# Performance work log

Measured on AMD Instinct MI355X. Metric: run time of the kernel, lower is better.

The kernel has to match this reference:

```python
import jax, jax.numpy as jnp
import numpy as np
from jax import lax

B, C, H, W = 4, 256, 64, 64
C8 = C // 8


def _conv1x1(x, w, b):
    # x: (B,C,H,W), w: (O,C) -> (B,O,H,W)
    return jnp.einsum('bchw,oc->bohw', x, w) + b[None, :, None, None]


def setup_inputs() -> dict:
    key = jax.random.key(0)
    ks = jax.random.split(key, 9)
    s1 = 1.0 / np.sqrt(C)          # fan-in scale for 1x1 convs
    sf = 1.0 / np.sqrt(2 * C * 9)  # fan-in scale for 3x3 conv
    return {
        'front_x':     jax.random.normal(ks[0], (B, C, H, W), jnp.float32),
        'cross_x':     jax.random.normal(ks[1], (B, C, H, W), jnp.float32),
        'front_x_hat': jax.random.normal(ks[2], (B, C, H, W), jnp.float32),
        'Wq': jax.random.normal(ks[3], (C8, C), jnp.float32) * s1,
        'bq': jnp.zeros((C8,), jnp.float32),
        'Wk': jax.random.normal(ks[4], (C8, C), jnp.float32) * s1,
        'bk': jnp.zeros((C8,), jnp.float32),
        'Wv': jax.random.normal(ks[5], (C, C), jnp.float32) * s1,
        'bv': jnp.zeros((C,), jnp.float32),
        'Wf': jax.random.normal(ks[6], (C, 2 * C, 3, 3), jnp.float32) * sf,
        'bf': jnp.zeros((C,), jnp.float32),
    }


def reference(front_x, cross_x, front_x_hat, Wq, bq, Wk, bk, Wv, bv, Wf, bf):
    b, c, h, w = front_x.shape
    hw = h * w
    # projections -> (B, C/8, HW)
    q = _conv1x1(cross_x, Wq, bq).reshape(b, -1, hw)
    k = _conv1x1(front_x, Wk, bk).reshape(b, -1, hw)
    # energy[b,i,j] = <key_i, query_j>  (B, HW, HW)
    energy = jnp.einsum('bci,bcj->bij', k, q)
    front_star = jnp.max(energy, axis=1)     # (B, HW) best key score per query
    front_arg = jnp.argmax(energy, axis=1)   # (B, HW) best key index per query
    # value projection and hard gather of best-matching value per position
    v = _conv1x1(front_x_hat, Wv, bv).reshape(b, c, hw)
    T = jnp.take_along_axis(v, front_arg[:, None, :], axis=2).reshape(b, c, h, w)
    S = front_star.reshape(b, 1, h, w)
    cat = jnp.concatenate([front_x, T], axis=1)  # (B, 2C, H, W)
    res = lax.conv_general_dilated(
        cat, Wf, window_strides=(1, 1), padding='SAME',
        dimension_numbers=('NCHW', 'OIHW', 'NCHW')) + bf[None, :, None, None]
    return front_x + res * S
```

## Files before the change

### kernel.cpp

```cpp
#include <hip/hip_runtime.h>

#define Bn 4
#define Cn 256
#define C8 32
#define Hn 64
#define Wn 64
#define HWn 4096
#define PADR 80
#define ROWS (HWn + 2 * PADR)
#define MARGIN 6e-3f

typedef __bf16 bf16x8 __attribute__((ext_vector_type(8)));
typedef float floatx4 __attribute__((ext_vector_type(4)));
typedef unsigned short u16x8 __attribute__((ext_vector_type(8)));

__device__ __forceinline__ unsigned short f2bf(float f) {
  union { float f; unsigned int u; } c; c.f = f;
  unsigned int u = c.u;
  return (unsigned short)((u + 0x7FFFu + ((u >> 16) & 1u)) >> 16);
}
__device__ __forceinline__ float bf2f(unsigned short h) {
  union { unsigned int u; float f; } c; c.u = ((unsigned int)h) << 16;
  return c.f;
}
__device__ __forceinline__ void gl_lds16(const void* g, void* l) {
  __builtin_amdgcn_global_load_lds(
      (__attribute__((address_space(1))) void*)(uintptr_t)g,
      (__attribute__((address_space(3))) void*)(uintptr_t)l, 16, 0, 0);
}

__global__ void prep_w(const float* __restrict__ Wq, const float* __restrict__ Wk,
                       const float* __restrict__ Wv, const float* __restrict__ Wf,
                       float* __restrict__ Wqf, float* __restrict__ Wkf,
                       unsigned short* __restrict__ Wvb, unsigned short* __restrict__ Wfb,
                       int* __restrict__ cnt) {
  size_t t = (size_t)blockIdx.x * 256 + threadIdx.x;
  if (t == 0) cnt[0] = 0;
  if (t < 8192) {
    int o = (int)(t / 256), c = (int)(t % 256);
    Wqf[(size_t)c * 32 + o] = Wq[t];
    Wkf[(size_t)c * 32 + o] = Wk[t];
  }
  if (t < 65536) Wvb[t] = f2bf(Wv[t]);
  if (t < (size_t)9 * 256 * 512) {
    int tap = (int)(t / (256 * 512));
    int rem = (int)(t % (256 * 512));
    int o = rem / 512, ci = rem % 512;
    Wfb[t] = f2bf(Wf[((size_t)o * 512 + ci) * 9 + tap]);
  }
}

__global__ __launch_bounds__(1024) void proj_qk(
    const float* __restrict__ cross_x, const float* __restrict__ front_x,
    const float* __restrict__ Wqf, const float* __restrict__ bq,
    const float* __restrict__ Wkf, const float* __restrict__ bk,
    float* __restrict__ qf, float* __restrict__ kf,
    unsigned short* __restrict__ qhi, unsigned short* __restrict__ qlo,
    unsigned short* __restrict__ khi, unsigned short* __restrict__ klo) {
  int tid = threadIdx.x;
  int lane = tid & 63, wv = tid >> 6;
  int slice = wv & 3;
  int chunk = wv >> 2;
  int j = blockIdx.x * 64 + lane;
  int b = blockIdx.y;
  int z = blockIdx.z;
  const float* x = (z == 0) ? cross_x : front_x;
  const float* Wg = (z == 0) ? Wqf : Wkf;
  const float* bd = (z == 0) ? bq : bk;
  float* outp = (z == 0) ? qf : kf;
  unsigned short* hip_ = (z == 0) ? qhi : khi;
  unsigned short* lop_ = (z == 0) ? qlo : klo;
  int o0 = slice * 8;
  int c0 = chunk * 64;

  __shared__ __align__(16) float Wl[8192];
  __shared__ float part[3 * 4 * 8 * 64];

  for (int u = tid; u < 8192; u += 1024) Wl[u] = Wg[u];
  __syncthreads();

  const float* xb = x + (size_t)b * Cn * HWn + j;
  floatx4 a0 = (floatx4)0.0f, a1 = (floatx4)0.0f;
#pragma unroll 16
  for (int c = c0; c < c0 + 64; ++c) {
    float xv = xb[(size_t)c * HWn];
    floatx4 wa = *reinterpret_cast<const floatx4*>(&Wl[c * 32 + o0]);
    floatx4 wb = *reinterpret_cast<const floatx4*>(&Wl[c * 32 + o0 + 4]);
    a0 += wa * xv;
    a1 += wb * xv;
  }
  if (chunk > 0) {
    float* dst = &part[(((chunk - 1) * 4 + slice) * 8) * 64];
#pragma unroll
    for (int o = 0; o < 4; ++o) { dst[o * 64 + lane] = a0[o]; dst[(o + 4) * 64 + lane] = a1[o]; }
  }
  __syncthreads();
  if (chunk != 0) return;
#pragma unroll
  for (int q = 0; q < 3; ++q) {
    const float* src = &part[((q * 4 + slice) * 8) * 64];
#pragma unroll
    for (int o = 0; o < 4; ++o) { a0[o] += src[o * 64 + lane]; a1[o] += src[(o + 4) * 64 + lane]; }
  }
  float acc[8];
#pragma unroll
  for (int o = 0; o < 4; ++o) { acc[o] = a0[o] + bd[o0 + o]; acc[o + 4] = a1[o] + bd[o0 + 4 + o]; }

  float* op = outp + ((size_t)b * HWn + j) * C8 + o0;
  u16x8 hv, lv;
#pragma unroll
  for (int o = 0; o < 8; ++o) {
    op[o] = acc[o];
    unsigned short h = f2bf(acc[o]);
    hv[o] = h;
    lv[o] = f2bf(acc[o] - bf2f(h));
  }
  *reinterpret_cast<u16x8*>(hip_ + ((size_t)b * HWn + j) * C8 + o0) = hv;
  *reinterpret_cast<u16x8*>(lop_ + ((size_t)b * HWn + j) * C8 + o0) = lv;
}

__global__ __launch_bounds__(1024, 8) void energy_cat(
    const unsigned short* __restrict__ khi, const unsigned short* __restrict__ klo,
    const unsigned short* __restrict__ qhi, const unsigned short* __restrict__ qlo,
    float* __restrict__ star, int* __restrict__ argb,
    int* __restrict__ cnt, int* __restrict__ list,
    const float* __restrict__ fx, const float* __restrict__ fxh,
    unsigned short* __restrict__ catC, unsigned short* __restrict__ xht) {
  int bx = blockIdx.x;
  if ((bx & 1) == 0) {
    int id = bx >> 1;
    int b = id >> 7;
    int j0 = (id & 127) * 32;
    int tid = threadIdx.x;
    int lane = tid & 63, wv = tid >> 6;
    int lm = lane & 15, lq = lane >> 4;

    __shared__ float bv1S[16][32];
    __shared__ int   bi1S[16][32];
    __shared__ float bv2S[16][32];

    bf16x8 qh[2], ql[2];
#pragma unroll
    for (int s = 0; s < 2; ++s) {
      int j = j0 + s * 16 + lm;
      qh[s] = *reinterpret_cast<const bf16x8*>(qhi + ((size_t)b * HWn + j) * 32 + lq * 8);
      ql[s] = *reinterpret_cast<const bf16x8*>(qlo + ((size_t)b * HWn + j) * 32 + lq * 8);
    }
    const unsigned short* kh_base = khi + (size_t)b * HWn * 32 + lq * 8;
    const unsigned short* kl_base = klo + (size_t)b * HWn * 32 + lq * 8;

    float b1[2], b2[2];
#pragma unroll
    for (int s = 0; s < 2; ++s) { b1[s] = -3.0e38f; b2[s] = -3.0e38f; }

    int ibase = wv * 256;
#pragma unroll 4
    for (int it = 0; it < 16; ++it) {
      int i0 = ibase + it * 16;
      bf16x8 ah = *reinterpret_cast<const bf16x8*>(kh_base + (size_t)(i0 + lm) * 32);
      bf16x8 al = *reinterpret_cast<const bf16x8*>(kl_base + (size_t)(i0 + lm) * 32);
#pragma unroll
      for (int s = 0; s < 2; ++s) {
        floatx4 acc = (floatx4)0.0f;
        acc = __builtin_amdgcn_mfma_f32_16x16x32_bf16(ah, qh[s], acc, 0, 0, 0);
        acc = __builtin_amdgcn_mfma_f32_16x16x32_bf16(ah, ql[s], acc, 0, 0, 0);
        acc = __builtin_amdgcn_mfma_f32_16x16x32_bf16(al, qh[s], acc, 0, 0, 0);
#pragma unroll
        for (int r = 0; r < 4; ++r) {
          unsigned code = (unsigned)(it * 4 + r);
          union { float f; unsigned u; } cv; cv.f = acc[r];
          cv.u = (cv.u & ~63u) | code;
          float vp = cv.f;
          b2[s] = __builtin_amdgcn_fmed3f(vp, b1[s], b2[s]);
          b1[s] = fmaxf(b1[s], vp);
        }
      }
    }
    int i1[2];
#pragma unroll
    for (int s = 0; s < 2; ++s) {
      union { float f; unsigned u; } cv; cv.f = b1[s];
      unsigned code = cv.u & 63u;
      i1[s] = ibase + (int)(code >> 2) * 16 + lq * 4 + (int)(code & 3u);
    }
#pragma unroll
    for (int s = 0; s < 2; ++s) {
#pragma unroll
      for (int m = 16; m <= 32; m <<= 1) {
        float ob1 = __shfl_xor(b1[s], m, 64);
        int oi1 = __shfl_xor(i1[s], m, 64);
        float ob2 = __shfl_xor(b2[s], m, 64);
        float c2;
        if (ob1 > b1[s] || (ob1 == b1[s] && oi1 < i1[s])) {
          c2 = fmaxf(b1[s], ob2);
          b1[s] = ob1; i1[s] = oi1;
        } else {
          c2 = fmaxf(ob1, b2[s]);
        }
        b2[s] = c2;
      }
      if (lq == 0) {
        bv1S[wv][s * 16 + lm] = b1[s];
        bi1S[wv][s * 16 + lm] = i1[s];
        bv2S[wv][s * 16 + lm] = b2[s];
      }
    }
    __syncthreads();
    if (tid < 32) {
      float B1 = bv1S[0][tid];
      int I1 = bi1S[0][tid];
      float B2 = bv2S[0][tid];
#pragma unroll
      for (int w = 1; w < 16; ++w) {
        float v1 = bv1S[w][tid];
        int ii = bi1S[w][tid];
        float v2 = bv2S[w][tid];
        if (v1 > B1) { B2 = fmaxf(B1, v2); B1 = v1; I1 = ii; }
        else B2 = fmaxf(B2, v1);
      }
      size_t o = (size_t)b * HWn + j0 + tid;
      union { float f; unsigned u; } cs; cs.f = B1;
      cs.u &= ~63u;
      star[o] = cs.f;
      argb[o] = I1;
      if (B1 - B2 < MARGIN) {
        int slot = atomicAdd(cnt, 1);
        list[slot] = (b << 12) | (j0 + (int)tid);
      }
    }
  } else {
    int id = bx >> 1;
    int j0 = (id & 63) * 64;
    int bz = id >> 6;
    int b = bz >> 1, which = bz & 1;
    int g4 = threadIdx.x >> 8;
    int tid = threadIdx.x & 255;
    int ci0 = g4 * 64;
    __shared__ unsigned short tile[4][64][66];

    const float* src = (which == 0) ? fx : fxh;
#pragma unroll
    for (int u = tid; u < 1024; u += 256) {
      int cl = u >> 4, h4 = (u & 15) * 4;
      floatx4 v = *reinterpret_cast<const floatx4*>(
          &src[((size_t)(b * Cn + ci0 + cl)) * HWn + j0 + h4]);
#pragma unroll
      for (int k = 0; k < 4; ++k) tile[g4][cl][h4 + k] = f2bf(v[k]);
    }
    __syncthreads();
#pragma unroll
    for (int u = tid; u < 512; u += 256) {
      int oct = u & 7, hw_l = u >> 3;
      u16x8 val;
#pragma unroll
      for (int k = 0; k < 8; ++k) val[k] = tile[g4][oct * 8 + k][hw_l];
      if (which == 0)
        *reinterpret_cast<u16x8*>(
            &catC[((size_t)b * ROWS + PADR + j0 + hw_l) * 512 + ci0 + oct * 8]) = val;
      else
        *reinterpret_cast<u16x8*>(
            &xht[((size_t)b * HWn + j0 + hw_l) * 256 + ci0 + oct * 8]) = val;
    }
  }
}

__global__ __launch_bounds__(256) void recheck_projv(
    const unsigned short* __restrict__ xht, const unsigned short* __restrict__ Wvb,
    const float* __restrict__ bv, unsigned short* __restrict__ vbf,
    const float* __restrict__ qf, const float* __restrict__ kf,
    const int* __restrict__ cnt, const int* __restrict__ list,
    float* __restrict__ star, int* __restrict__ argb) {
  int bx = blockIdx.x;
  if ((bx & 1) == 0) {
    int id = bx >> 1;
    int m0 = (id & 31) * 128;
    int o0 = ((id >> 5) & 1) * 128;
    int b = id >> 6;
    int tid = threadIdx.x;
    int lane = tid & 63, wv = tid >> 6;
    int wm = wv >> 1, wn = wv & 1;
    int lm = lane & 15, lq = lane >> 4;

    union SMu {
      struct { unsigned short A[2][128 * 32]; unsigned short B[2][128 * 32]; } st;
      unsigned short TS[128 * 136];
    };
    __shared__ __align__(16) SMu sm;

    floatx4 acc[4][4];
#pragma unroll
    for (int im = 0; im < 4; ++im)
#pragma unroll
      for (int in = 0; in < 4; ++in) acc[im][in] = (floatx4)0.0f;

    const int srow = lane >> 2;
    const int soff = (((lane & 3) ^ ((lane >> 3) & 3)) * 8);
    const int sa = (lq ^ ((lm >> 1) & 3)) * 8;
    const unsigned short* ag = Wvb + (size_t)o0 * 256;
    const unsigned short* bg = xht + ((size_t)b * HWn + m0) * 256;

    auto STAGE = [&](int buf, int kc) {
#pragma unroll
      for (int i = 0; i < 2; ++i) {
        int r0 = wv * 32 + i * 16;
        gl_lds16(ag + ((size_t)(r0 + srow)) * 256 + kc + soff, &sm.st.A[buf][r0 * 32]);
        gl_lds16(bg + ((size_t)(r0 + srow)) * 256 + kc + soff, &sm.st.B[buf][r0 * 32]);
      }
    };
    auto COMPUTE = [&](int buf) {
      bf16x8 afr[4];
#pragma unroll
      for (int im = 0; im < 4; ++im)
        afr[im] = *reinterpret_cast<const bf16x8*>(
            &sm.st.A[buf][(wm * 64 + im * 16 + lm) * 32 + sa]);
#pragma unroll
      for (int in = 0; in < 4; ++in) {
        bf16x8 bfr = *reinterpret_cast<const bf16x8*>(
            &sm.st.B[buf][(wn * 64 + in * 16 + lm) * 32 + sa]);
#pragma unroll
        for (int im = 0; im < 4; ++im)
          acc[im][in] = __builtin_amdgcn_mfma_f32_16x16x32_bf16(
              afr[im], bfr, acc[im][in], 0, 0, 0);
      }
    };

    STAGE(0, 0);
#pragma unroll 2
    for (int st = 0; st < 8; ++st) {
      __builtin_amdgcn_s_barrier();
      if (st < 7) {
        STAGE((st + 1) & 1, (st + 1) * 32);
        asm volatile("s_waitcnt vmcnt(4)" ::: "memory");
      } else {
        asm volatile("s_waitcnt vmcnt(0)" ::: "memory");
      }
      __builtin_amdgcn_s_barrier();
      __builtin_amdgcn_sched_barrier(0);
      COMPUTE(st & 1);
    }
    __builtin_amdgcn_s_barrier();

#pragma unroll
    for (int in = 0; in < 4; ++in) {
      int pl = wn * 64 + in * 16 + lm;
#pragma unroll
      for (int im = 0; im < 4; ++im) {
#pragma unroll
        for (int r = 0; r < 4; ++r) {
          int ol = wm * 64 + im * 16 + lq * 4 + r;
          sm.TS[pl * 136 + ol] = f2bf(acc[im][in][r] + bv[o0 + ol]);
        }
      }
    }
    __syncthreads();
    for (int idx = tid; idx < 128 * 16; idx += 256) {
      int p = idx >> 4, ch = idx & 15;
      u16x8 val = *reinterpret_cast<const u16x8*>(&sm.TS[p * 136 + ch * 8]);
      *reinterpret_cast<u16x8*>(
          &vbf[((size_t)b * HWn + m0 + p) * 256 + o0 + ch * 8]) = val;
    }
  } else {
    __shared__ double bvS[4];
    __shared__ int biS[4];
    int n = cnt[0];
    int tid = threadIdx.x;
    int lane = tid & 63, wv = tid >> 6;
    for (int idx = bx >> 1; idx < n; idx += 256) {
      int e = list[idx];
      int b = e >> 12, j = e & 4095;
      const float* qp = qf + ((size_t)b * HWn + j) * 32;
      double qj[32];
#pragma unroll
      for (int o = 0; o < 32; ++o) qj[o] = (double)qp[o];
      double best = -1.0e300;
      int bi = 1 << 30;
      for (int i = tid; i < HWn; i += 256) {
        const float* kp = kf + ((size_t)b * HWn + i) * 32;
        double s = 0.0;
#pragma unroll
        for (int o = 0; o < 32; ++o) s += (double)kp[o] * qj[o];
        if (s > best) { best = s; bi = i; }
      }
#pragma unroll
      for (int m = 1; m < 64; m <<= 1) {
        double ob = __shfl_xor(best, m, 64);
        int oi = __shfl_xor(bi, m, 64);
        if (ob > best || (ob == best && oi < bi)) { best = ob; bi = oi; }
      }
      if (lane == 0) { bvS[wv] = best; biS[wv] = bi; }
      __syncthreads();
      if (tid == 0) {
#pragma unroll
        for (int w = 1; w < 4; ++w) {
          if (bvS[w] > best || (bvS[w] == best && biS[w] < bi)) {
            best = bvS[w]; bi = biS[w];
          }
        }
        star[(size_t)b * HWn + j] = (float)best;
        argb[(size_t)b * HWn + j] = bi;
      }
      __syncthreads();
    }
  }
}

__global__ __launch_bounds__(256) void gather_cat(
    const unsigned short* __restrict__ vbf, const int* __restrict__ argb,
    unsigned short* __restrict__ catC) {
  int b = blockIdx.y;
  int tid = threadIdx.x;
  if (blockIdx.x == 16) {
    for (int u = tid; u < 2 * PADR * 512; u += 256) {
      int r = u >> 9;
      int rr = (r < PADR) ? r : (HWn + r);
      catC[((size_t)b * ROWS + rr) * 512 + (u & 511)] = 0;
    }
    return;
  }
  __shared__ int ajS[256];
  int j0 = blockIdx.x * 256;
  ajS[tid] = argb[(size_t)b * HWn + j0 + tid];
  __syncthreads();
#pragma unroll 4
  for (int u = tid; u < 256 * 32; u += 256) {
    int pl = u >> 5, ch = u & 31;
    int aj = ajS[pl];
    u16x8 val = *reinterpret_cast<const u16x8*>(
        &vbf[((size_t)b * HWn + aj) * 256 + ch * 8]);
    *reinterpret_cast<u16x8*>(
        &catC[((size_t)b * ROWS + PADR + j0 + pl) * 512 + 256 + ch * 8]) = val;
  }
}

__global__ __launch_bounds__(256) void conv_mfma(
    const unsigned short* __restrict__ catC, const unsigned short* __restrict__ Wfb,
    unsigned short* __restrict__ Pg) {
  int m0 = blockIdx.x * 128;
  int o0 = blockIdx.y * 128;
  int bz = blockIdx.z;
  int b = bz / 3, g = bz % 3;
  int dy = g - 1;
  int tid = threadIdx.x;
  int lane = tid & 63;
  int wv = tid >> 6;
  int wm = wv >> 1, wn = wv & 1;
  int lm = lane & 15, lq = lane >> 4;
  const bool lane_first = (lm == 0);
  const bool lane_last = (lm == 15);

  __shared__ __align__(16) unsigned short AS[2][3 * 128 * 32];
  __shared__ __align__(16) unsigned short BS[2][144 * 32];

  floatx4 acc[4][4];
#pragma unroll
  for (int im = 0; im < 4; ++im)
#pragma unroll
    for (int in = 0; in < 4; ++in) acc[im][in] = (floatx4)0.0f;

  const int srow = lane >> 2;
  const int soff = (((lane & 3) ^ ((lane >> 3) & 3)) * 8);
  const int sa = (lq ^ ((lm >> 1) & 3)) * 8;
  const unsigned short* bg =
      catC + ((size_t)b * ROWS + PADR + m0 + dy * 64 - 1) * 512;
  const unsigned short* ag = Wfb + ((size_t)(g * 3) * 256 + o0) * 512;

  auto STAGE = [&](unsigned short* ASb, unsigned short* BSb, int kc) {
    if (wv < 3) {
      const unsigned short* at = ag + (size_t)wv * 256 * 512;
#pragma unroll
      for (int s = 0; s < 8; ++s)
        gl_lds16(at + ((size_t)(s * 16 + srow)) * 512 + kc + soff,
                 &ASb[(wv * 128 + s * 16) * 32]);
    } else {
#pragma unroll
      for (int s = 0; s < 9; ++s)
        gl_lds16(bg + ((size_t)(s * 16 + srow)) * 512 + kc + soff,
                 &BSb[(s * 16) * 32]);
    }
  };
  auto COMPUTE = [&](const unsigned short* ASb, const unsigned short* BSb) {
#pragma unroll
    for (int t = 0; t < 3; ++t) {
      bf16x8 afr[4];
#pragma unroll
      for (int im = 0; im < 4; ++im)
        afr[im] = *reinterpret_cast<const bf16x8*>(
            &ASb[(t * 128 + wm * 64 + im * 16 + lm) * 32 + sa]);
#pragma unroll
      for (int in = 0; in < 4; ++in) {
        int u = wn * 64 + in * 16 + lm + t;
        int sb = (lq ^ ((u >> 1) & 3)) * 8;
        u16x8 braw = *reinterpret_cast<const u16x8*>(&BSb[u * 32 + sb]);
        if ((t == 0 && in == 0 && lane_first) ||
            (t == 2 && in == 3 && lane_last))
          braw = (u16x8)(unsigned short)0;
        union { u16x8 u8; bf16x8 h; } cvt; cvt.u8 = braw;
#pragma unroll
        for (int im = 0; im < 4; ++im)
          acc[im][in] = __builtin_amdgcn_mfma_f32_16x16x32_bf16(
              afr[im], cvt.h, acc[im][in], 0, 0, 0);
      }
    }
  };

  STAGE(AS[0], BS[0], 0);
  __syncthreads();
  for (int kci = 0; kci < 16; kci += 2) {
    if (kci < 15) STAGE(AS[1], BS[1], (kci + 1) * 32);
    COMPUTE(AS[0], BS[0]);
    __syncthreads();
    if (kci < 14) STAGE(AS[0], BS[0], (kci + 2) * 32);
    COMPUTE(AS[1], BS[1]);
    __syncthreads();
  }

  unsigned short* P = Pg + ((size_t)(g * Bn + b) * Cn) * HWn;
#pragma unroll
  for (int in = 0; in < 4; ++in) {
    int p = m0 + wn * 64 + in * 16 + lm;
#pragma unroll
    for (int im = 0; im < 4; ++im) {
      int ob = o0 + wm * 64 + im * 16 + lq * 4;
#pragma unroll
      for (int r = 0; r < 4; ++r)
        P[(size_t)(ob + r) * HWn + p] = f2bf(acc[im][in][r]);
    }
  }
}

__global__ __launch_bounds__(256) void combine(
    const unsigned short* __restrict__ Pg, const float* __restrict__ fx,
    const float* __restrict__ bf, const float* __restrict__ star,
    float* __restrict__ out) {
  size_t e = ((size_t)blockIdx.x * 256 + threadIdx.x) * 8;
  int p = (int)(e & 4095);
  int bo = (int)(e >> 12);
  int o = bo & 255, b = bo >> 8;
  const size_t gs = (size_t)Bn * Cn * HWn;
  u16x8 q0 = *reinterpret_cast<const u16x8*>(Pg + e);
  u16x8 q1 = *reinterpret_cast<const u16x8*>(Pg + gs + e);
  u16x8 q2 = *reinterpret_cast<const u16x8*>(Pg + 2 * gs + e);
  float bias = bf[o];
  const float* sp = star + (size_t)b * HWn + p;
  const float* fp = fx + e;
  float* op = out + e;
#pragma unroll
  for (int h = 0; h < 2; ++h) {
    floatx4 s = *reinterpret_cast<const floatx4*>(sp + h * 4);
    floatx4 f = *reinterpret_cast<const floatx4*>(fp + h * 4);
    floatx4 r;
#pragma unroll
    for (int i = 0; i < 4; ++i) {
      int k = h * 4 + i;
      float a = bf2f(q0[k]) + bf2f(q1[k]) + bf2f(q2[k]);
      r[i] = f[i] + (a + bias) * s[i];
    }
    *reinterpret_cast<floatx4*>(op + h * 4) = r;
  }
}

extern "C" void kernel_launch(void* const* d_in, const int* in_sizes, int n_in,
                              void* d_out, int out_size, void* d_ws, size_t ws_size,
                              hipStream_t stream) {
  const float* front_x   = (const float*)d_in[0];
  const float* cross_x   = (const float*)d_in[1];
  const float* front_hat = (const float*)d_in[2];
  const float* Wq = (const float*)d_in[3];
  const float* bq = (const float*)d_in[4];
  const float* Wk = (const float*)d_in[5];
  const float* bk = (const float*)d_in[6];
  const float* Wv = (const float*)d_in[7];
  const float* bv = (const float*)d_in[8];
  const float* Wf = (const float*)d_in[9];
  const float* bf = (const float*)d_in[10];
  float* out = (float*)d_out;

  char* ws = (char*)d_ws;
  size_t off = 0;
  auto alloc = [&](size_t bytes) -> void* {
    void* p = (void*)(ws + off);
    off += (bytes + 255) & ~(size_t)255;
    return p;
  };
  float* Wqf = (float*)alloc(8192 * sizeof(float));
  float* Wkf = (float*)alloc(8192 * sizeof(float));
  unsigned short* Wvb = (unsigned short*)alloc(65536 * sizeof(unsigned short));
  unsigned short* Wfb = (unsigned short*)alloc((size_t)9 * 256 * 512 * sizeof(unsigned short));
  float* qf  = (float*)alloc((size_t)Bn * HWn * C8 * sizeof(float));
  float* kf  = (float*)alloc((size_t)Bn * HWn * C8 * sizeof(float));
  unsigned short* qhi = (unsigned short*)alloc((size_t)Bn * HWn * C8 * 2);
  unsigned short* qlo = (unsigned short*)alloc((size_t)Bn * HWn * C8 * 2);
  unsigned short* khi = (unsigned short*)alloc((size_t)Bn * HWn * C8 * 2);
  unsigned short* klo = (unsigned short*)alloc((size_t)Bn * HWn * C8 * 2);
  float*  star = (float*)alloc((size_t)Bn * HWn * sizeof(float));
  int*    argb = (int*)alloc((size_t)Bn * HWn * sizeof(int));
  int*    cnt  = (int*)alloc(256);
  int*    list = (int*)alloc((size_t)Bn * HWn * sizeof(int));
  unsigned short* xht = (unsigned short*)alloc((size_t)Bn * HWn * 256 * 2);
  unsigned short* vbf = (unsigned short*)alloc((size_t)Bn * HWn * 256 * 2);
  unsigned short* catC = (unsigned short*)alloc((size_t)Bn * ROWS * 512 * sizeof(unsigned short));
  unsigned short* Pg = (unsigned short*)alloc((size_t)3 * Bn * Cn * HWn * 2);

  prep_w<<<dim3((9 * 256 * 512 + 255) / 256), dim3(256), 0, stream>>>(
      Wq, Wk, Wv, Wf, Wqf, Wkf, Wvb, Wfb, cnt);

  proj_qk<<<dim3(HWn / 64, Bn, 2), dim3(1024), 0, stream>>>(
      cross_x, front_x, Wqf, bq, Wkf, bk, qf, kf, qhi, qlo, khi, klo);

  energy_cat<<<dim3(1024), dim3(1024), 0, stream>>>(
      khi, klo, qhi, qlo, star, argb, cnt, list,
      front_x, front_hat, catC, xht);

  recheck_projv<<<dim3(512), dim3(256), 0, stream>>>(
      xht, Wvb, bv, vbf, qf, kf, cnt, list, star, argb);

  gather_cat<<<dim3(HWn / 256 + 1, Bn), dim3(256), 0, stream>>>(vbf, argb, catC);

  conv_mfma<<<dim3(HWn / 128, Cn / 128, Bn * 3), dim3(256), 0, stream>>>(
      catC, Wfb, Pg);

  combine<<<dim3((Bn * Cn * HWn / 8) / 256), dim3(256), 0, stream>>>(
      Pg, front_x, bf, star, out);
}
```

Measured before the change: 238.5 us.

## Fuse value gather into conv loads and merge weight prep into projection

Drops the gather_cat kernel. The conv B-operand loader now reads the front_x half from a 256-wide padded buffer and fetches gathered value rows directly through argmax-indexed pointers, with a zero row for out-of-range taps. The separate prep_w kernel is folded into the Q/K projection launch as extra blocks, and the projection reads the raw weight transpose itself. This removes two launches and the write and re-read of the 512-wide concatenated buffer, at the cost of scattered row loads inside the conv staging.

```diff
diff --git a/kernel.cpp b/kernel.cpp
--- a/kernel.cpp
+++ b/kernel.cpp
@@ -29,43 +29,48 @@
       (__attribute__((address_space(3))) void*)(uintptr_t)l, 16, 0, 0);
 }
 
-__global__ void prep_w(const float* __restrict__ Wq, const float* __restrict__ Wk,
-                       const float* __restrict__ Wv, const float* __restrict__ Wf,
-                       float* __restrict__ Wqf, float* __restrict__ Wkf,
-                       unsigned short* __restrict__ Wvb, unsigned short* __restrict__ Wfb,
-                       int* __restrict__ cnt) {
-  size_t t = (size_t)blockIdx.x * 256 + threadIdx.x;
-  if (t == 0) cnt[0] = 0;
-  if (t < 8192) {
-    int o = (int)(t / 256), c = (int)(t % 256);
-    Wqf[(size_t)c * 32 + o] = Wq[t];
-    Wkf[(size_t)c * 32 + o] = Wk[t];
-  }
-  if (t < 65536) Wvb[t] = f2bf(Wv[t]);
-  if (t < (size_t)9 * 256 * 512) {
-    int tap = (int)(t / (256 * 512));
-    int rem = (int)(t % (256 * 512));
-    int o = rem / 512, ci = rem % 512;
-    Wfb[t] = f2bf(Wf[((size_t)o * 512 + ci) * 9 + tap]);
-  }
-}
-
-__global__ __launch_bounds__(1024) void proj_qk(
+__global__ __launch_bounds__(1024) void proj_prep(
     const float* __restrict__ cross_x, const float* __restrict__ front_x,
-    const float* __restrict__ Wqf, const float* __restrict__ bq,
-    const float* __restrict__ Wkf, const float* __restrict__ bk,
+    const float* __restrict__ Wq, const float* __restrict__ bq,
+    const float* __restrict__ Wk, const float* __restrict__ bk,
+    const float* __restrict__ Wv, const float* __restrict__ Wf,
     float* __restrict__ qf, float* __restrict__ kf,
     unsigned short* __restrict__ qhi, unsigned short* __restrict__ qlo,
-    unsigned short* __restrict__ khi, unsigned short* __restrict__ klo) {
+    unsigned short* __restrict__ khi, unsigned short* __restrict__ klo,
+    unsigned short* __restrict__ Wvb, unsigned short* __restrict__ Wfb,
+    unsigned short* __restrict__ catF, unsigned short* __restrict__ zpad,
+    int* __restrict__ cnt) {
+  int bx = blockIdx.x;
   int tid = threadIdx.x;
+  if (bx >= 512) {
+    size_t t = (size_t)(bx - 512) * 1024 + tid;
+    if (t == 0) cnt[0] = 0;
+    if (t < 256) zpad[t] = 0;
+    if (t < 163840) {
+      int col = (int)(t & 255);
+      int r4 = (int)(t >> 8);
+      int bb = r4 / 160, rr = r4 % 160;
+      int row = (rr < PADR) ? rr : (HWn + rr);
+      catF[((size_t)bb * ROWS + row) * 256 + col] = 0;
+    }
+    if (t < 65536) Wvb[t] = f2bf(Wv[t]);
+    {
+      int tap = (int)(t / (256 * 512));
+      int rem = (int)(t % (256 * 512));
+      int o = rem / 512, ci = rem % 512;
+      Wfb[t] = f2bf(Wf[((size_t)o * 512 + ci) * 9 + tap]);
+    }
+    return;
+  }
   int lane = tid & 63, wv = tid >> 6;
   int slice = wv & 3;
   int chunk = wv >> 2;
-  int j = blockIdx.x * 64 + lane;
-  int b = blockIdx.y;
-  int z = blockIdx.z;
+  int jb = bx & 63;
+  int b = (bx >> 6) & 3;
+  int z = bx >> 8;
+  int j = jb * 64 + lane;
   const float* x = (z == 0) ? cross_x : front_x;
-  const float* Wg = (z == 0) ? Wqf : Wkf;
+  const float* Wraw = (z == 0) ? Wq : Wk;
   const float* bd = (z == 0) ? bq : bk;
   float* outp = (z == 0) ? qf : kf;
   unsigned short* hip_ = (z == 0) ? qhi : khi;
@@ -76,7 +81,10 @@
   __shared__ __align__(16) float Wl[8192];
   __shared__ float part[3 * 4 * 8 * 64];
 
-  for (int u = tid; u < 8192; u += 1024) Wl[u] = Wg[u];
+  for (int u = tid; u < 8192; u += 1024) {
+    int c = u >> 5, o = u & 31;
+    Wl[u] = Wraw[o * 256 + c];
+  }
   __syncthreads();
 
   const float* xb = x + (size_t)b * Cn * HWn + j;
@@ -125,7 +133,7 @@
     float* __restrict__ star, int* __restrict__ argb,
     int* __restrict__ cnt, int* __restrict__ list,
     const float* __restrict__ fx, const float* __restrict__ fxh,
-    unsigned short* __restrict__ catC, unsigned short* __restrict__ xht) {
+    unsigned short* __restrict__ catF, unsigned short* __restrict__ xht) {
   int bx = blockIdx.x;
   if ((bx & 1) == 0) {
     int id = bx >> 1;
@@ -256,7 +264,7 @@
       for (int k = 0; k < 8; ++k) val[k] = tile[g4][oct * 8 + k][hw_l];
       if (which == 0)
         *reinterpret_cast<u16x8*>(
-            &catC[((size_t)b * ROWS + PADR + j0 + hw_l) * 512 + ci0 + oct * 8]) = val;
+            &catF[((size_t)b * ROWS + PADR + j0 + hw_l) * 256 + ci0 + oct * 8]) = val;
       else
         *reinterpret_cast<u16x8*>(
             &xht[((size_t)b * HWn + j0 + hw_l) * 256 + ci0 + oct * 8]) = val;
@@ -404,37 +412,10 @@
   }
 }
 
-__global__ __launch_bounds__(256) void gather_cat(
+__global__ __launch_bounds__(256) void conv_mfma(
+    const unsigned short* __restrict__ catF, const unsigned short* __restrict__ Wfb,
     const unsigned short* __restrict__ vbf, const int* __restrict__ argb,
-    unsigned short* __restrict__ catC) {
-  int b = blockIdx.y;
-  int tid = threadIdx.x;
-  if (blockIdx.x == 16) {
-    for (int u = tid; u < 2 * PADR * 512; u += 256) {
-      int r = u >> 9;
-      int rr = (r < PADR) ? r : (HWn + r);
-      catC[((size_t)b * ROWS + rr) * 512 + (u & 511)] = 0;
-    }
-    return;
-  }
-  __shared__ int ajS[256];
-  int j0 = blockIdx.x * 256;
-  ajS[tid] = argb[(size_t)b * HWn + j0 + tid];
-  __syncthreads();
-#pragma unroll 4
-  for (int u = tid; u < 256 * 32; u += 256) {
-    int pl = u >> 5, ch = u & 31;
-    int aj = ajS[pl];
-    u16x8 val = *reinterpret_cast<const u16x8*>(
-        &vbf[((size_t)b * HWn + aj) * 256 + ch * 8]);
-    *reinterpret_cast<u16x8*>(
-        &catC[((size_t)b * ROWS + PADR + j0 + pl) * 512 + 256 + ch * 8]) = val;
-  }
-}
-
-__global__ __launch_bounds__(256) void conv_mfma(
-    const unsigned short* __restrict__ catC, const unsigned short* __restrict__ Wfb,
-    unsigned short* __restrict__ Pg) {
+    const unsigned short* __restrict__ zpad, unsigned short* __restrict__ Pg) {
   int m0 = blockIdx.x * 128;
   int o0 = blockIdx.y * 128;
   int bz = blockIdx.z;
@@ -460,9 +441,23 @@
   const int srow = lane >> 2;
   const int soff = (((lane & 3) ^ ((lane >> 3) & 3)) * 8);
   const int sa = (lq ^ ((lm >> 1) & 3)) * 8;
-  const unsigned short* bg =
-      catC + ((size_t)b * ROWS + PADR + m0 + dy * 64 - 1) * 512;
+  const unsigned short* catb =
+      catF + ((size_t)b * ROWS + PADR + m0 + dy * 64 - 1) * 256;
   const unsigned short* ag = Wfb + ((size_t)(g * 3) * 256 + o0) * 512;
+
+  const unsigned short* tsrc[9];
+#pragma unroll
+  for (int s = 0; s < 9; ++s) tsrc[s] = zpad;
+  if (wv == 3) {
+    int p0 = m0 + dy * 64 - 1 + srow;
+#pragma unroll
+    for (int s = 0; s < 9; ++s) {
+      int p = p0 + s * 16;
+      bool v = ((unsigned)p < (unsigned)HWn);
+      int aj = v ? argb[(size_t)b * HWn + (v ? p : 0)] : 0;
+      tsrc[s] = v ? (vbf + ((size_t)b * HWn + aj) * 256) : zpad;
+    }
+  }
 
   auto STAGE = [&](unsigned short* ASb, unsigned short* BSb, int kc) {
     if (wv < 3) {
@@ -471,11 +466,16 @@
       for (int s = 0; s < 8; ++s)
         gl_lds16(at + ((size_t)(s * 16 + srow)) * 512 + kc + soff,
                  &ASb[(wv * 128 + s * 16) * 32]);
+    } else if (kc < 256) {
+#pragma unroll
+      for (int s = 0; s < 9; ++s)
+        gl_lds16(catb + ((size_t)(s * 16 + srow)) * 256 + kc + soff,
+                 &BSb[(s * 16) * 32]);
     } else {
+      int kk = kc - 256;
 #pragma unroll
       for (int s = 0; s < 9; ++s)
-        gl_lds16(bg + ((size_t)(s * 16 + srow)) * 512 + kc + soff,
-                 &BSb[(s * 16) * 32]);
+        gl_lds16(tsrc[s] + kk + soff, &BSb[(s * 16) * 32]);
     }
   };
   auto COMPUTE = [&](const unsigned short* ASb, const unsigned short* BSb) {
@@ -582,8 +582,6 @@
     off += (bytes + 255) & ~(size_t)255;
     return p;
   };
-  float* Wqf = (float*)alloc(8192 * sizeof(float));
-  float* Wkf = (float*)alloc(8192 * sizeof(float));
   unsigned short* Wvb = (unsigned short*)alloc(65536 * sizeof(unsigned short));
   unsigned short* Wfb = (unsigned short*)alloc((size_t)9 * 256 * 512 * sizeof(unsigned short));
   float* qf  = (float*)alloc((size_t)Bn * HWn * C8 * sizeof(float));
@@ -598,26 +596,23 @@
   int*    list = (int*)alloc((size_t)Bn * HWn * sizeof(int));
   unsigned short* xht = (unsigned short*)alloc((size_t)Bn * HWn * 256 * 2);
   unsigned short* vbf = (unsigned short*)alloc((size_t)Bn * HWn * 256 * 2);
-  unsigned short* catC = (unsigned short*)alloc((size_t)Bn * ROWS * 512 * sizeof(unsigned short));
+  unsigned short* catF = (unsigned short*)alloc((size_t)Bn * ROWS * 256 * sizeof(unsigned short));
+  unsigned short* zpad = (unsigned short*)alloc(256 * sizeof(unsigned short));
   unsigned short* Pg = (unsigned short*)alloc((size_t)3 * Bn * Cn * HWn * 2);
 
-  prep_w<<<dim3((9 * 256 * 512 + 255) / 256), dim3(256), 0, stream>>>(
-      Wq, Wk, Wv, Wf, Wqf, Wkf, Wvb, Wfb, cnt);
-
-  proj_qk<<<dim3(HWn / 64, Bn, 2), dim3(1024), 0, stream>>>(
-      cross_x, front_x, Wqf, bq, Wkf, bk, qf, kf, qhi, qlo, khi, klo);
+  proj_prep<<<dim3(512 + 1152), dim3(1024), 0, stream>>>(
+      cross_x, front_x, Wq, bq, Wk, bk, Wv, Wf,
+      qf, kf, qhi, qlo, khi, klo, Wvb, Wfb, catF, zpad, cnt);
 
   energy_cat<<<dim3(1024), dim3(1024), 0, stream>>>(
       khi, klo, qhi, qlo, star, argb, cnt, list,
-      front_x, front_hat, catC, xht);
+      front_x, front_hat, catF, xht);
 
   recheck_projv<<<dim3(512), dim3(256), 0, stream>>>(
       xht, Wvb, bv, vbf, qf, kf, cnt, list, star, argb);
 
-  gather_cat<<<dim3(HWn / 256 + 1, Bn), dim3(256), 0, stream>>>(vbf, argb, catC);
-
   conv_mfma<<<dim3(HWn / 128, Cn / 128, Bn * 3), dim3(256), 0, stream>>>(
-      catC, Wfb, Pg);
+      catF, Wfb, vbf, argb, zpad, Pg);
 
   combine<<<dim3((Bn * Cn * HWn / 8) / 256), dim3(256), 0, stream>>>(
       Pg, front_x, bf, star, out);
```

New measurement: 239.1 us. Within noise of the previous version (+0.2%).
